# Optimization experiments

Hardware: AMD Instinct MI355X
Metric: run time of the kernel (lower is better)

## Reference

```python
import jax, jax.numpy as jnp
import numpy as np

D_MODEL = 256
NHEAD = 8
HEAD_DIM = D_MODEL // NHEAD
NLAYERS = 8
LAYER_NAMES = ('self', 'cross', 'self', 'cross', 'self', 'cross', 'self', 'cross')
LN_EPS = 1e-5
ATTN_EPS = 1e-6


def _layernorm(x, g, b):
    mu = jnp.mean(x, axis=-1, keepdims=True)
    var = jnp.mean(jnp.square(x - mu), axis=-1, keepdims=True)
    return (x - mu) * jax.lax.rsqrt(var + LN_EPS) * g + b


def _encoder_layer(x, source, Wq, Wk, Wv, Wm, W1, W2, g1, b1, g2, b2):
    # x: [N, L, C], source: [N, S, C]; weights stored [in, out] so y = x @ W
    bs, L, C = x.shape
    S = source.shape[1]
    q = (x @ Wq).reshape(bs, L, NHEAD, HEAD_DIM)
    k = (source @ Wk).reshape(bs, S, NHEAD, HEAD_DIM)
    v = (source @ Wv).reshape(bs, S, NHEAD, HEAD_DIM)
    # LoFTR LinearAttention: feature map elu(x)+1, O(N d^2) kernelized attention
    Q = jax.nn.elu(q) + 1.0
    K = jax.nn.elu(k) + 1.0
    v_n = v / S  # normalize values by kv length for numerical stability
    KV = jnp.einsum('nshd,nshv->nhdv', K, v_n)            # [N,H,D,D]
    Z = 1.0 / (jnp.einsum('nlhd,nhd->nlh', Q, K.sum(axis=1)) + ATTN_EPS)
    msg = jnp.einsum('nlhd,nhdv,nlh->nlhv', Q, KV, Z) * S  # [N,L,H,D]
    msg = msg.reshape(bs, L, C) @ Wm
    msg = _layernorm(msg, g1, b1)
    h = jnp.concatenate([x, msg], axis=-1)                 # [N,L,2C]
    h = jax.nn.relu(h @ W1) @ W2
    h = _layernorm(h, g2, b2)
    return x + h


def _transformer(feat0, feat1, Wq, Wk, Wv, Wm, W1, W2, g1, b1, g2, b2):
    for i, name in enumerate(LAYER_NAMES):
        p = (Wq[i], Wk[i], Wv[i], Wm[i], W1[i], W2[i], g1[i], b1[i], g2[i], b2[i])
        if name == 'self':
            feat0 = _encoder_layer(feat0, feat0, *p)
            feat1 = _encoder_layer(feat1, feat1, *p)
        else:  # cross
            new0 = _encoder_layer(feat0, feat1, *p)
            feat1 = _encoder_layer(feat1, feat0, *p)
            feat0 = new0
    return feat0, feat1


def setup_inputs() -> dict:
    key = jax.random.key(0)
    ks = jax.random.split(key, 8)
    N, L = 4, 4800
    feat0 = jax.random.normal(ks[0], (N, L, D_MODEL), jnp.float32)
    feat1 = jax.random.normal(ks[1], (N, L, D_MODEL), jnp.float32)
    xav = lambda k, fi, fo: jax.random.normal(k, (NLAYERS, fi, fo), jnp.float32) * float(np.sqrt(2.0 / (fi + fo)))
    Wq = xav(ks[2], D_MODEL, D_MODEL)
    Wk = xav(ks[3], D_MODEL, D_MODEL)
    Wv = xav(ks[4], D_MODEL, D_MODEL)
    Wm = xav(ks[5], D_MODEL, D_MODEL)
    W1 = xav(ks[6], 2 * D_MODEL, 2 * D_MODEL)
    W2 = xav(ks[7], 2 * D_MODEL, D_MODEL)
    g1 = jnp.ones((NLAYERS, D_MODEL), jnp.float32)
    b1 = jnp.zeros((NLAYERS, D_MODEL), jnp.float32)
    g2 = jnp.ones((NLAYERS, D_MODEL), jnp.float32)
    b2 = jnp.zeros((NLAYERS, D_MODEL), jnp.float32)
    return dict(feat0=feat0, feat1=feat1, Wq=Wq, Wk=Wk, Wv=Wv, Wm=Wm,
                W1=W1, W2=W2, g1=g1, b1=b1, g2=g2, b2=b2)


def reference(feat0, feat1, Wq, Wk, Wv, Wm, W1, W2, g1, b1, g2, b2):
    return _transformer(feat0, feat1, Wq, Wk, Wv, Wm, W1, W2, g1, b1, g2, b2)
```

## Files before the change

### kernel.cpp

```cpp
#include <hip/hip_runtime.h>
#include <math.h>

#define RTOT 19200
#define RALL 38400
#define CDIM 256
#define SLEN 4800
#define NB 8
#define NHEAD 8
#define SEG 25
#define SCHUNK 192

typedef __attribute__((ext_vector_type(8))) short short8v;
typedef __attribute__((ext_vector_type(4))) float f32x4;

__device__ __forceinline__ ushort f2b(float f) {
    unsigned u = __float_as_uint(f);
    unsigned r = (u + 0x7FFFu + ((u >> 16) & 1u)) >> 16;
    return (ushort)r;
}
__device__ __forceinline__ float b2f(ushort u) {
    return __uint_as_float(((unsigned)u) << 16);
}

__device__ __forceinline__ float elu1(float v) { return v > 0.0f ? v + 1.0f : __expf(v); }

__device__ __forceinline__ void gload16(const void* g, void* l) {
    __builtin_amdgcn_global_load_lds((const __attribute__((address_space(1))) void*)g,
                                     (__attribute__((address_space(3))) void*)l, 16, 0, 0);
}

__global__ __launch_bounds__(256) void qkv_gemm(
    const ushort* __restrict__ A, const ushort* __restrict__ Bt,
    ushort* __restrict__ Oq, ushort* __restrict__ Ok, ushort* __restrict__ Ov)
{
    __shared__ __align__(16) ushort As[2][128 * 32];
    __shared__ __align__(16) ushort Bs[2][128 * 32];
    const int t = threadIdx.x;
    const int wave = t >> 6, lane = t & 63;
    const int bm = blockIdx.y * 128, bn = blockIdx.x * 128;
    const int wr = wave >> 1, wc = wave & 1;
    const int lr = lane & 15, lk = (lane >> 4) * 8;

    const int srow = t >> 2;
    const int sgrp = ((t & 3) * 8) ^ ((srow & 3) * 8);
    const ushort* bAr = A + (size_t)(bm + srow) * 256 + sgrp;
    const ushort* bBr = Bt + (size_t)(bn + srow) * 256 + sgrp;

    const f32x4 z4 = {0.f, 0.f, 0.f, 0.f};
    f32x4 acc[4][4];
    #pragma unroll
    for (int m = 0; m < 4; ++m)
        #pragma unroll
        for (int n = 0; n < 4; ++n) acc[m][n] = z4;

    auto stage = [&](int k0, int b) {
        char* la = (char*)As[b] + wave * 1024;
        char* lb = (char*)Bs[b] + wave * 1024;
        gload16(bAr + k0, la);
        gload16(bAr + k0 + 64 * 256, la + 4096);
        gload16(bBr + k0, lb);
        gload16(bBr + k0 + 64 * 256, lb + 4096);
    };

    stage(0, 0);
    __syncthreads();
    int cur = 0;
    for (int k0 = 0; k0 < 256; k0 += 32) {
        if (k0 + 32 < 256) stage(k0 + 32, cur ^ 1);
        short8v af[4], bfr[4];
        #pragma unroll
        for (int m = 0; m < 4; ++m) {
            const int r = wr * 64 + m * 16 + lr;
            af[m] = *(const short8v*)&As[cur][r * 32 + (lk ^ ((r & 3) * 8))];
        }
        #pragma unroll
        for (int n = 0; n < 4; ++n) {
            const int r = wc * 64 + n * 16 + lr;
            bfr[n] = *(const short8v*)&Bs[cur][r * 32 + (lk ^ ((r & 3) * 8))];
        }
        #pragma unroll
        for (int m = 0; m < 4; ++m)
            #pragma unroll
            for (int n = 0; n < 4; ++n)
                acc[m][n] = __builtin_amdgcn_mfma_f32_16x16x32_bf16(af[m], bfr[n], acc[m][n], 0, 0, 0);
        __syncthreads();
        cur ^= 1;
    }

    const int orow = bm + wr * 64 + (lane >> 4) * 4;
    const int ocol = bn + wc * 64 + lr;
    #pragma unroll
    for (int m = 0; m < 4; ++m)
        #pragma unroll
        for (int n = 0; n < 4; ++n)
            #pragma unroll
            for (int j = 0; j < 4; ++j) {
                const float v = acc[m][n][j];
                const size_t row = (size_t)(orow + m * 16 + j);
                const int col = ocol + n * 16;
                const int seg = col >> 8, c = col & 255;
                ushort* dst = seg == 0 ? Oq : (seg == 1 ? Ok : Ov);
                dst[row * 256 + c] = f2b(seg < 2 ? elu1(v) : v);
            }
}

__global__ __launch_bounds__(256) void w1_gemm(
    const ushort* __restrict__ A, const ushort* __restrict__ A2,
    const ushort* __restrict__ Bt, ushort* __restrict__ O)
{
    __shared__ __align__(16) ushort As[2][128 * 32];
    __shared__ __align__(16) ushort Bs[2][128 * 32];
    const int t = threadIdx.x;
    const int wave = t >> 6, lane = t & 63;
    const int bm = blockIdx.y * 128, bn = blockIdx.x * 128;
    const int wr = wave >> 1, wc = wave & 1;
    const int lr = lane & 15, lk = (lane >> 4) * 8;

    const int srow = t >> 2;
    const int sgrp = ((t & 3) * 8) ^ ((srow & 3) * 8);
    const ushort* bAr = A + (size_t)(bm + srow) * 256 + sgrp;
    const ushort* bA2r = A2 + (size_t)(bm + srow) * 256 + sgrp;
    const ushort* bBr = Bt + (size_t)(bn + srow) * 512 + sgrp;

    const f32x4 z4 = {0.f, 0.f, 0.f, 0.f};
    f32x4 acc[4][4];
    #pragma unroll
    for (int m = 0; m < 4; ++m)
        #pragma unroll
        for (int n = 0; n < 4; ++n) acc[m][n] = z4;

    auto stage = [&](int k0, int b) {
        char* la = (char*)As[b] + wave * 1024;
        char* lb = (char*)Bs[b] + wave * 1024;
        const ushort* ga = (k0 < 256) ? (bAr + k0) : (bA2r + (k0 - 256));
        gload16(ga, la);
        gload16(ga + 64 * 256, la + 4096);
        gload16(bBr + k0, lb);
        gload16(bBr + k0 + (size_t)64 * 512, lb + 4096);
    };

    stage(0, 0);
    __syncthreads();
    int cur = 0;
    for (int k0 = 0; k0 < 512; k0 += 32) {
        if (k0 + 32 < 512) stage(k0 + 32, cur ^ 1);
        short8v af[4], bfr[4];
        #pragma unroll
        for (int m = 0; m < 4; ++m) {
            const int r = wr * 64 + m * 16 + lr;
            af[m] = *(const short8v*)&As[cur][r * 32 + (lk ^ ((r & 3) * 8))];
        }
        #pragma unroll
        for (int n = 0; n < 4; ++n) {
            const int r = wc * 64 + n * 16 + lr;
            bfr[n] = *(const short8v*)&Bs[cur][r * 32 + (lk ^ ((r & 3) * 8))];
        }
        #pragma unroll
        for (int m = 0; m < 4; ++m)
            #pragma unroll
            for (int n = 0; n < 4; ++n)
                acc[m][n] = __builtin_amdgcn_mfma_f32_16x16x32_bf16(af[m], bfr[n], acc[m][n], 0, 0, 0);
        __syncthreads();
        cur ^= 1;
    }

    const int orow = bm + wr * 64 + (lane >> 4) * 4;
    const int ocol = bn + wc * 64 + lr;
    #pragma unroll
    for (int m = 0; m < 4; ++m)
        #pragma unroll
        for (int n = 0; n < 4; ++n)
            #pragma unroll
            for (int j = 0; j < 4; ++j) {
                const float v = acc[m][n][j];
                O[(size_t)(orow + m * 16 + j) * 512 + ocol + n * 16] = f2b(v > 0.f ? v : 0.f);
            }
}

__global__ __launch_bounds__(256) void gemm_ln32(
    const ushort* __restrict__ A, int lda,
    const ushort* __restrict__ Bt,
    const float* __restrict__ g, const float* __restrict__ bb,
    const float* __restrict__ rx0, const float* __restrict__ rx1,
    float* __restrict__ outf, ushort* __restrict__ outb, int K)
{
    __shared__ __align__(16) ushort As[2][32 * 32];
    __shared__ __align__(16) ushort Bs[2][256 * 32];
    __shared__ float red[2][4][32];
    const int t = threadIdx.x;
    const int wave = t >> 6, lane = t & 63;
    const int bm = blockIdx.x * 32;
    const int lr = lane & 15, kg = lane >> 4, lk = kg * 8;

    const int srow = t >> 2;
    const int sg = ((t & 3) * 8) ^ ((srow & 3) * 8);
    const ushort* aP = A + (size_t)(bm + srow) * lda + sg;
    const ushort* bP = Bt + (size_t)srow * K + sg;
    const size_t b64 = (size_t)64 * K;

    auto stage = [&](int k0, int b) {
        if (srow < 32) gload16(aP + k0, (char*)As[b] + wave * 1024);
        char* lb = (char*)Bs[b] + wave * 1024;
        gload16(bP + k0, lb);
        gload16(bP + k0 + b64, lb + 4096);
        gload16(bP + k0 + 2 * b64, lb + 8192);
        gload16(bP + k0 + 3 * b64, lb + 12288);
    };

    const f32x4 z4 = {0.f, 0.f, 0.f, 0.f};
    f32x4 acc[2][4];
    #pragma unroll
    for (int m = 0; m < 2; ++m)
        #pragma unroll
        for (int n = 0; n < 4; ++n) acc[m][n] = z4;

    stage(0, 0);
    __syncthreads();
    int cur = 0;
    for (int k0 = 0; k0 < K; k0 += 32) {
        if (k0 + 32 < K) stage(k0 + 32, cur ^ 1);
        short8v af[2], bfr[4];
        #pragma unroll
        for (int m = 0; m < 2; ++m) {
            const int r = m * 16 + lr;
            af[m] = *(const short8v*)&As[cur][r * 32 + (lk ^ ((r & 3) * 8))];
        }
        #pragma unroll
        for (int n = 0; n < 4; ++n) {
            const int r = wave * 64 + n * 16 + lr;
            bfr[n] = *(const short8v*)&Bs[cur][r * 32 + (lk ^ ((r & 3) * 8))];
        }
        #pragma unroll
        for (int m = 0; m < 2; ++m)
            #pragma unroll
            for (int n = 0; n < 4; ++n)
                acc[m][n] = __builtin_amdgcn_mfma_f32_16x16x32_bf16(af[m], bfr[n], acc[m][n], 0, 0, 0);
        __syncthreads();
        cur ^= 1;
    }

    #pragma unroll
    for (int m = 0; m < 2; ++m)
        #pragma unroll
        for (int j = 0; j < 4; ++j) {
            float s = 0.f, q = 0.f;
            #pragma unroll
            for (int n = 0; n < 4; ++n) { const float v = acc[m][n][j]; s += v; q += v * v; }
            #pragma unroll
            for (int mk = 1; mk < 16; mk <<= 1) { s += __shfl_xor(s, mk); q += __shfl_xor(q, mk); }
            if (lr == 0) {
                red[0][wave][m * 16 + kg * 4 + j] = s;
                red[1][wave][m * 16 + kg * 4 + j] = q;
            }
        }
    __syncthreads();

    float gv[4], bv[4];
    #pragma unroll
    for (int n = 0; n < 4; ++n) {
        const int col = wave * 64 + n * 16 + lr;
        gv[n] = g[col]; bv[n] = bb[col];
    }
    const float* rxb = (bm < RTOT) ? rx0 + (size_t)bm * CDIM : rx1 + (size_t)(bm - RTOT) * CDIM;

    #pragma unroll
    for (int m = 0; m < 2; ++m)
        #pragma unroll
        for (int j = 0; j < 4; ++j) {
            const int row = m * 16 + kg * 4 + j;
            const float tot = red[0][0][row] + red[0][1][row] + red[0][2][row] + red[0][3][row];
            const float tq  = red[1][0][row] + red[1][1][row] + red[1][2][row] + red[1][3][row];
            const float mu = tot * (1.0f / 256.0f);
            const float var = tq * (1.0f / 256.0f) - mu * mu;
            const float inv = rsqrtf(var + 1e-5f);
            const size_t go = (size_t)(bm + row) * CDIM;
            #pragma unroll
            for (int n = 0; n < 4; ++n) {
                const int col = wave * 64 + n * 16 + lr;
                float val = (acc[m][n][j] - mu) * inv * gv[n] + bv[n];
                val += rxb[(size_t)row * CDIM + col];
                outf[go + col] = val;
                outb[go + col] = f2b(val);
            }
        }
}

__global__ __launch_bounds__(256) void attn_wm_ln(
    const ushort* __restrict__ Qb, const ushort* __restrict__ KVbT,
    const ushort* __restrict__ Ksb, const ushort* __restrict__ WmT,
    const float* __restrict__ g, const float* __restrict__ bb,
    ushort* __restrict__ mln, int xorv)
{
    __shared__ __align__(16) ushort Ms[32 * 256];
    __shared__ __align__(16) ushort Bs[2][256 * 32];
    __shared__ float red[2][4][32];
    const int t = threadIdx.x, wave = t >> 6, lane = t & 63;
    const int bm = blockIdx.x * 32;
    const int n = bm / SLEN, src = n ^ xorv;
    const int lr = lane & 15, kg = lane >> 4, lk = kg * 8;
    const f32x4 z4 = {0.f, 0.f, 0.f, 0.f};

    const int srow = t >> 2;
    const int sg = ((t & 3) * 8) ^ ((srow & 3) * 8);
    const ushort* bP = WmT + (size_t)srow * 256 + sg;
    auto stageB = [&](int k0, int b) {
        char* lb = (char*)Bs[b] + wave * 1024;
        gload16(bP + k0, lb);
        gload16(bP + k0 + 64 * 256, lb + 4096);
        gload16(bP + k0 + 128 * 256, lb + 8192);
        gload16(bP + k0 + 192 * 256, lb + 12288);
    };
    stageB(0, 0);

    {
        const int rw = (wave & 1) * 16;
        const size_t qrow = ((size_t)bm + rw + lr) * CDIM;
        char* mb = (char*)Ms;
        for (int h = (wave >> 1); h < NHEAD; h += 2) {
            const short8v af = *(const short8v*)&Qb[qrow + h * 32 + kg * 8];
            const ushort* bbp = KVbT + ((size_t)(src * NHEAD + h)) * 1024;
            const short8v b0 = *(const short8v*)&bbp[lr * 32 + kg * 8];
            const short8v b1 = *(const short8v*)&bbp[(16 + lr) * 32 + kg * 8];
            const short8v bz = *(const short8v*)&Ksb[((size_t)(src * NHEAD + h)) * 512 + lr * 32 + kg * 8];
            f32x4 a0 = __builtin_amdgcn_mfma_f32_16x16x32_bf16(af, b0, z4, 0, 0, 0);
            f32x4 a1 = __builtin_amdgcn_mfma_f32_16x16x32_bf16(af, b1, z4, 0, 0, 0);
            f32x4 az = __builtin_amdgcn_mfma_f32_16x16x32_bf16(af, bz, z4, 0, 0, 0);
            #pragma unroll
            for (int j = 0; j < 4; ++j) {
                const float zj = __shfl(az[j], lane & 48);
                const float rz = 1.0f / (zj + 1e-6f);
                const int orow = rw + kg * 4 + j;
                const int swz = (orow & 7) << 4;
                *(ushort*)(mb + ((orow * 512 + (h * 32 + lr) * 2) ^ swz)) = f2b(a0[j] * rz);
                *(ushort*)(mb + ((orow * 512 + (h * 32 + 16 + lr) * 2) ^ swz)) = f2b(a1[j] * rz);
            }
        }
    }
    __syncthreads();

    f32x4 acc[2][4];
    #pragma unroll
    for (int m = 0; m < 2; ++m)
        #pragma unroll
        for (int nn = 0; nn < 4; ++nn) acc[m][nn] = z4;

    int cur = 0;
    for (int k0 = 0; k0 < 256; k0 += 32) {
        if (k0 + 32 < 256) stageB(k0 + 32, cur ^ 1);
        short8v af[2], bfr[4];
        #pragma unroll
        for (int m = 0; m < 2; ++m) {
            const int r = m * 16 + lr;
            af[m] = *(const short8v*)((char*)Ms + ((r * 512 + k0 * 2 + kg * 16) ^ ((r & 7) << 4)));
        }
        #pragma unroll
        for (int nn = 0; nn < 4; ++nn) {
            const int r = wave * 64 + nn * 16 + lr;
            bfr[nn] = *(const short8v*)&Bs[cur][r * 32 + (lk ^ ((r & 3) * 8))];
        }
        #pragma unroll
        for (int m = 0; m < 2; ++m)
            #pragma unroll
            for (int nn = 0; nn < 4; ++nn)
                acc[m][nn] = __builtin_amdgcn_mfma_f32_16x16x32_bf16(af[m], bfr[nn], acc[m][nn], 0, 0, 0);
        __syncthreads();
        cur ^= 1;
    }

    #pragma unroll
    for (int m = 0; m < 2; ++m)
        #pragma unroll
        for (int j = 0; j < 4; ++j) {
            float s = 0.f, q = 0.f;
            #pragma unroll
            for (int nn = 0; nn < 4; ++nn) { const float v = acc[m][nn][j]; s += v; q += v * v; }
            #pragma unroll
            for (int mk = 1; mk < 16; mk <<= 1) { s += __shfl_xor(s, mk); q += __shfl_xor(q, mk); }
            if (lr == 0) {
                red[0][wave][m * 16 + kg * 4 + j] = s;
                red[1][wave][m * 16 + kg * 4 + j] = q;
            }
        }
    __syncthreads();

    float gv[4], bv[4];
    #pragma unroll
    for (int nn = 0; nn < 4; ++nn) {
        const int col = wave * 64 + nn * 16 + lr;
        gv[nn] = g[col]; bv[nn] = bb[col];
    }
    #pragma unroll
    for (int m = 0; m < 2; ++m)
        #pragma unroll
        for (int j = 0; j < 4; ++j) {
            const int row = m * 16 + kg * 4 + j;
            const float tot = red[0][0][row] + red[0][1][row] + red[0][2][row] + red[0][3][row];
            const float tq  = red[1][0][row] + red[1][1][row] + red[1][2][row] + red[1][3][row];
            const float mu = tot * (1.0f / 256.0f);
            const float var = tq * (1.0f / 256.0f) - mu * mu;
            const float inv = rsqrtf(var + 1e-5f);
            const size_t go = (size_t)(bm + row) * CDIM;
            #pragma unroll
            for (int nn = 0; nn < 4; ++nn) {
                const int col = wave * 64 + nn * 16 + lr;
                mln[go + col] = f2b((acc[m][nn][j] - mu) * inv * gv[nn] + bv[nn]);
            }
        }
}

__global__ __launch_bounds__(256) void wconv_t(
    const float* __restrict__ src, ushort* __restrict__ dst, int R, int C, size_t dstride)
{
    __shared__ float tile[32][33];
    const int l = blockIdx.z;
    const int r0 = blockIdx.y * 32, c0 = blockIdx.x * 32;
    const int tx = threadIdx.x & 31, ty = threadIdx.x >> 5;
    const float* s = src + (size_t)l * R * C;
    ushort* d = dst + (size_t)l * dstride;
    for (int i = ty; i < 32; i += 8) tile[i][tx] = s[(size_t)(r0 + i) * C + c0 + tx];
    __syncthreads();
    for (int i = ty; i < 32; i += 8) d[(size_t)(c0 + i) * R + r0 + tx] = f2b(tile[tx][i]);
}

__global__ __launch_bounds__(256) void kv_part_k(
    const ushort* __restrict__ Kb, const ushort* __restrict__ Vb,
    float* __restrict__ KVp, float* __restrict__ Ksp)
{
    const int blk = blockIdx.x;
    const int seg = blk % SEG;
    const int h = (blk / SEG) % NHEAD;
    const int n = blk / (SEG * NHEAD);
    const int s0 = seg * SCHUNK;
    __shared__ float Ks[16][32];
    __shared__ float Vs[16][32];
    const int t = threadIdx.x;
    const int rr = t >> 4, c2 = (t & 15) * 2;
    const int d = t >> 3, v0 = (t & 7) * 4;
    float a0 = 0, a1 = 0, a2 = 0, a3 = 0, ksum = 0;
    for (int c = 0; c < SCHUNK; c += 16) {
        const size_t off = ((size_t)(n * SLEN + s0 + c + rr)) * CDIM + h * 32 + c2;
        const ushort2 ku = *(const ushort2*)&Kb[off];
        const ushort2 vu = *(const ushort2*)&Vb[off];
        Ks[rr][c2] = b2f(ku.x); Ks[rr][c2 + 1] = b2f(ku.y);
        Vs[rr][c2] = b2f(vu.x); Vs[rr][c2 + 1] = b2f(vu.y);
        __syncthreads();
        #pragma unroll
        for (int q = 0; q < 16; ++q) {
            const float kd = Ks[q][d];
            a0 += kd * Vs[q][v0 + 0];
            a1 += kd * Vs[q][v0 + 1];
            a2 += kd * Vs[q][v0 + 2];
            a3 += kd * Vs[q][v0 + 3];
        }
        if (t < 32) {
            #pragma unroll
            for (int q = 0; q < 16; ++q) ksum += Ks[q][t];
        }
        __syncthreads();
    }
    float* kvp = KVp + ((size_t)((n * NHEAD + h) * SEG + seg)) * 1024;
    kvp[t * 4 + 0] = a0;
    kvp[t * 4 + 1] = a1;
    kvp[t * 4 + 2] = a2;
    kvp[t * 4 + 3] = a3;
    if (t < 32) Ksp[((size_t)((n * NHEAD + h) * SEG + seg)) * 32 + t] = ksum;
}

__global__ __launch_bounds__(256) void kv_reduce_k(
    const float* __restrict__ KVp, const float* __restrict__ Ksp,
    ushort* __restrict__ KVbT, ushort* __restrict__ Ksb)
{
    const int nh = blockIdx.x;
    const int t = threadIdx.x;
    #pragma unroll
    for (int i = 0; i < 4; ++i) {
        const int idx = t * 4 + i;
        const int v = idx >> 5, d = idx & 31;
        float s = 0;
        for (int seg = 0; seg < SEG; ++seg)
            s += KVp[((size_t)(nh * SEG + seg)) * 1024 + d * 32 + v];
        KVbT[(size_t)nh * 1024 + idx] = f2b(s);
    }
    #pragma unroll
    for (int i = 0; i < 2; ++i) {
        const int idx = t * 2 + i;
        const int c = idx >> 5, d = idx & 31;
        float s = 0;
        if (c == 0)
            for (int seg = 0; seg < SEG; ++seg)
                s += Ksp[((size_t)(nh * SEG + seg)) * 32 + d];
        Ksb[(size_t)nh * 512 + idx] = f2b(s);
    }
}

__global__ __launch_bounds__(256) void cvt_in_k(const float* __restrict__ src, ushort* __restrict__ dst) {
    const size_t i = ((size_t)blockIdx.x * 256 + threadIdx.x) * 4;
    const float4 v = *(const float4*)&src[i];
    ushort4 ob = make_ushort4(f2b(v.x), f2b(v.y), f2b(v.z), f2b(v.w));
    *(ushort4*)&dst[i] = ob;
}

struct Ws {
    float *xf, *KVp, *Ksp;
    ushort *xb, *Qb, *Kb, *Vb, *h1b, *KVbT, *Ksb;
    ushort *WqkvT, *WmT, *W1T, *W2T;
};

static void layer_pass(const float* rx0, const float* rx1, float* destf, int xorv,
                       const ushort* WqkvT, const ushort* WmT,
                       const ushort* W1T, const ushort* W2T,
                       const float* g1, const float* b1,
                       const float* g2, const float* b2,
                       const Ws& w, hipStream_t stream)
{
    const dim3 blk(256);
    qkv_gemm<<<dim3(6, RALL / 128), blk, 0, stream>>>(w.xb, WqkvT, w.Qb, w.Kb, w.Vb);
    kv_part_k<<<dim3(NB * NHEAD * SEG), blk, 0, stream>>>(w.Kb, w.Vb, w.KVp, w.Ksp);
    kv_reduce_k<<<dim3(NB * NHEAD), blk, 0, stream>>>(w.KVp, w.Ksp, w.KVbT, w.Ksb);
    attn_wm_ln<<<dim3(RALL / 32), blk, 0, stream>>>(
        w.Qb, w.KVbT, w.Ksb, WmT, g1, b1, w.Kb, xorv);
    w1_gemm<<<dim3(4, RALL / 128), blk, 0, stream>>>(w.xb, w.Kb, W1T, w.h1b);
    gemm_ln32<<<dim3(RALL / 32), blk, 0, stream>>>(
        w.h1b, 512, W2T, g2, b2, rx0, rx1, destf, w.xb, 512);
}

extern "C" void kernel_launch(void* const* d_in, const int* in_sizes, int n_in,
                              void* d_out, int out_size, void* d_ws, size_t ws_size,
                              hipStream_t stream) {
    (void)in_sizes; (void)n_in; (void)out_size; (void)ws_size;
    const float* f0in = (const float*)d_in[0];
    const float* f1in = (const float*)d_in[1];
    const float* WqA = (const float*)d_in[2];
    const float* WkA = (const float*)d_in[3];
    const float* WvA = (const float*)d_in[4];
    const float* WmA = (const float*)d_in[5];
    const float* W1A = (const float*)d_in[6];
    const float* W2A = (const float*)d_in[7];
    const float* g1A = (const float*)d_in[8];
    const float* b1A = (const float*)d_in[9];
    const float* g2A = (const float*)d_in[10];
    const float* b2A = (const float*)d_in[11];

    float* outf = (float*)d_out;
    const size_t RC = (size_t)RTOT * CDIM;
    const size_t RAC = (size_t)RALL * CDIM;

    float* wsf = (float*)d_ws;
    Ws w;
    w.xf  = wsf;
    w.KVp = w.xf + RAC;
    w.Ksp = w.KVp + (size_t)64 * SEG * 1024;
    ushort* p = (ushort*)(w.Ksp + 64 * SEG * 32);
    w.xb = p;   p += RAC;
    w.Qb = p;   p += RAC;
    w.Kb = p;   p += RAC;
    w.Vb = p;   p += RAC;
    w.h1b = p;  p += (size_t)RALL * 512;
    w.KVbT = p; p += 64 * 1024;
    w.Ksb = p;  p += 64 * 512;
    w.WqkvT = p; p += (size_t)8 * 768 * 256;
    w.WmT = p;  p += (size_t)8 * 256 * 256;
    w.W1T = p;  p += (size_t)8 * 512 * 512;
    w.W2T = p;  p += (size_t)8 * 512 * 256;

    const dim3 blk(256);
    wconv_t<<<dim3(8, 8, 8), blk, 0, stream>>>(WqA, w.WqkvT,             256, 256, 768 * 256);
    wconv_t<<<dim3(8, 8, 8), blk, 0, stream>>>(WkA, w.WqkvT + 256 * 256, 256, 256, 768 * 256);
    wconv_t<<<dim3(8, 8, 8), blk, 0, stream>>>(WvA, w.WqkvT + 512 * 256, 256, 256, 768 * 256);
    wconv_t<<<dim3(8, 8, 8), blk, 0, stream>>>(WmA, w.WmT, 256, 256, 65536);
    wconv_t<<<dim3(16, 16, 8), blk, 0, stream>>>(W1A, w.W1T, 512, 512, 262144);
    wconv_t<<<dim3(8, 16, 8), blk, 0, stream>>>(W2A, w.W2T, 512, 256, 131072);

    cvt_in_k<<<dim3(RC / 1024), blk, 0, stream>>>(f0in, w.xb);
    cvt_in_k<<<dim3(RC / 1024), blk, 0, stream>>>(f1in, w.xb + RC);

    for (int l = 0; l < 8; ++l) {
        const int xorv = (l & 1) ? 4 : 0;
        const float* rx0 = (l == 0) ? f0in : w.xf;
        const float* rx1 = (l == 0) ? f1in : w.xf + RC;
        float* destf = (l == 7) ? outf : w.xf;
        layer_pass(rx0, rx1, destf, xorv,
                   w.WqkvT + (size_t)l * 768 * 256,
                   w.WmT + (size_t)l * 65536,
                   w.W1T + (size_t)l * 262144,
                   w.W2T + (size_t)l * 131072,
                   g1A + l * 256, b1A + l * 256, g2A + l * 256, b2A + l * 256,
                   w, stream);
    }
}
```

Before: 1.439 ms.

## Keep residual stream in bf16 only and stage full A rows in LDS for FFN GEMMs

Drops the fp32 residual copy: the W2+LayerNorm kernel now reads the residual from the bf16 activation buffer and writes fp32 output only on the last layer, which cuts fp32 read/write traffic per layer. The W1 GEMM moves to 64-row tiles that load the whole 512-wide A row (x concatenated with the message) into swizzled LDS once, and the W2 kernel does the same with a 32-row A block, so only B is double-buffered. The cost is that the residual accumulates in bf16 across all eight layers, which loses precision, and the W1 kernel now uses more LDS with a smaller M tile.

```diff
diff --git a/kernel.cpp b/kernel.cpp
--- a/kernel.cpp
+++ b/kernel.cpp
@@ -104,59 +104,61 @@
             }
 }
 
-__global__ __launch_bounds__(256) void w1_gemm(
-    const ushort* __restrict__ A, const ushort* __restrict__ A2,
+__global__ __launch_bounds__(256) void w1_gemm64(
+    const ushort* __restrict__ xb, const ushort* __restrict__ mln,
     const ushort* __restrict__ Bt, ushort* __restrict__ O)
 {
-    __shared__ __align__(16) ushort As[2][128 * 32];
+    __shared__ __align__(16) ushort A512[64 * 512];
     __shared__ __align__(16) ushort Bs[2][128 * 32];
-    const int t = threadIdx.x;
-    const int wave = t >> 6, lane = t & 63;
-    const int bm = blockIdx.y * 128, bn = blockIdx.x * 128;
+    const int t = threadIdx.x, wave = t >> 6, lane = t & 63;
+    const int bm = blockIdx.y * 64, bn = blockIdx.x * 128;
     const int wr = wave >> 1, wc = wave & 1;
-    const int lr = lane & 15, lk = (lane >> 4) * 8;
+    const int lr = lane & 15, kg = lane >> 4, lk = kg * 8;
+    const f32x4 z4 = {0.f, 0.f, 0.f, 0.f};
+
+    #pragma unroll
+    for (int i = 0; i < 16; ++i) {
+        const int row = i * 4 + wave;
+        const int gl = lane ^ (row & 7);
+        const ushort* src = (gl < 32) ? (xb + (size_t)(bm + row) * 256 + gl * 8)
+                                      : (mln + (size_t)(bm + row) * 256 + (gl - 32) * 8);
+        gload16(src, (char*)A512 + row * 1024);
+    }
 
     const int srow = t >> 2;
-    const int sgrp = ((t & 3) * 8) ^ ((srow & 3) * 8);
-    const ushort* bAr = A + (size_t)(bm + srow) * 256 + sgrp;
-    const ushort* bA2r = A2 + (size_t)(bm + srow) * 256 + sgrp;
-    const ushort* bBr = Bt + (size_t)(bn + srow) * 512 + sgrp;
-
-    const f32x4 z4 = {0.f, 0.f, 0.f, 0.f};
-    f32x4 acc[4][4];
-    #pragma unroll
-    for (int m = 0; m < 4; ++m)
+    const int sg = ((t & 3) * 8) ^ ((srow & 3) * 8);
+    const ushort* bP = Bt + (size_t)(bn + srow) * 512 + sg;
+    auto stageB = [&](int k0, int b) {
+        char* lb = (char*)Bs[b] + wave * 1024;
+        gload16(bP + k0, lb);
+        gload16(bP + k0 + (size_t)64 * 512, lb + 4096);
+    };
+
+    f32x4 acc[2][4];
+    #pragma unroll
+    for (int m = 0; m < 2; ++m)
         #pragma unroll
         for (int n = 0; n < 4; ++n) acc[m][n] = z4;
 
-    auto stage = [&](int k0, int b) {
-        char* la = (char*)As[b] + wave * 1024;
-        char* lb = (char*)Bs[b] + wave * 1024;
-        const ushort* ga = (k0 < 256) ? (bAr + k0) : (bA2r + (k0 - 256));
-        gload16(ga, la);
-        gload16(ga + 64 * 256, la + 4096);
-        gload16(bBr + k0, lb);
-        gload16(bBr + k0 + (size_t)64 * 512, lb + 4096);
-    };
-
-    stage(0, 0);
+    stageB(0, 0);
     __syncthreads();
     int cur = 0;
     for (int k0 = 0; k0 < 512; k0 += 32) {
-        if (k0 + 32 < 512) stage(k0 + 32, cur ^ 1);
-        short8v af[4], bfr[4];
-        #pragma unroll
-        for (int m = 0; m < 4; ++m) {
-            const int r = wr * 64 + m * 16 + lr;
-            af[m] = *(const short8v*)&As[cur][r * 32 + (lk ^ ((r & 3) * 8))];
+        if (k0 + 32 < 512) stageB(k0 + 32, cur ^ 1);
+        short8v af[2], bfr[4];
+        #pragma unroll
+        for (int m = 0; m < 2; ++m) {
+            const int r = wr * 32 + m * 16 + lr;
+            const int q = (k0 >> 3) + kg;
+            af[m] = *(const short8v*)((char*)A512 + r * 1024 + ((q ^ (r & 7)) << 4));
         }
         #pragma unroll
         for (int n = 0; n < 4; ++n) {
-            const int r = wc * 64 + n * 16 + lr;
-            bfr[n] = *(const short8v*)&Bs[cur][r * 32 + (lk ^ ((r & 3) * 8))];
-        }
-        #pragma unroll
-        for (int m = 0; m < 4; ++m)
+            const int rB = wc * 64 + n * 16 + lr;
+            bfr[n] = *(const short8v*)&Bs[cur][rB * 32 + (lk ^ ((rB & 3) * 8))];
+        }
+        #pragma unroll
+        for (int m = 0; m < 2; ++m)
             #pragma unroll
             for (int n = 0; n < 4; ++n)
                 acc[m][n] = __builtin_amdgcn_mfma_f32_16x16x32_bf16(af[m], bfr[n], acc[m][n], 0, 0, 0);
@@ -164,10 +166,10 @@
         cur ^= 1;
     }
 
-    const int orow = bm + wr * 64 + (lane >> 4) * 4;
+    const int orow = bm + wr * 32 + kg * 4;
     const int ocol = bn + wc * 64 + lr;
     #pragma unroll
-    for (int m = 0; m < 4; ++m)
+    for (int m = 0; m < 2; ++m)
         #pragma unroll
         for (int n = 0; n < 4; ++n)
             #pragma unroll
@@ -177,58 +179,62 @@
             }
 }
 
-__global__ __launch_bounds__(256) void gemm_ln32(
-    const ushort* __restrict__ A, int lda,
+__global__ __launch_bounds__(256) void w2_ln(
+    const ushort* __restrict__ A,
     const ushort* __restrict__ Bt,
     const float* __restrict__ g, const float* __restrict__ bb,
-    const float* __restrict__ rx0, const float* __restrict__ rx1,
-    float* __restrict__ outf, ushort* __restrict__ outb, int K)
-{
-    __shared__ __align__(16) ushort As[2][32 * 32];
+    const ushort* __restrict__ resid,
+    float* __restrict__ outf,
+    ushort* __restrict__ outb)
+{
+    __shared__ __align__(16) ushort A512[32 * 512];
     __shared__ __align__(16) ushort Bs[2][256 * 32];
     __shared__ float red[2][4][32];
-    const int t = threadIdx.x;
-    const int wave = t >> 6, lane = t & 63;
+    const int t = threadIdx.x, wave = t >> 6, lane = t & 63;
     const int bm = blockIdx.x * 32;
     const int lr = lane & 15, kg = lane >> 4, lk = kg * 8;
+    const f32x4 z4 = {0.f, 0.f, 0.f, 0.f};
+
+    #pragma unroll
+    for (int i = 0; i < 8; ++i) {
+        const int row = i * 4 + wave;
+        const int gl = lane ^ (row & 7);
+        gload16(A + (size_t)(bm + row) * 512 + gl * 8, (char*)A512 + row * 1024);
+    }
 
     const int srow = t >> 2;
     const int sg = ((t & 3) * 8) ^ ((srow & 3) * 8);
-    const ushort* aP = A + (size_t)(bm + srow) * lda + sg;
-    const ushort* bP = Bt + (size_t)srow * K + sg;
-    const size_t b64 = (size_t)64 * K;
-
-    auto stage = [&](int k0, int b) {
-        if (srow < 32) gload16(aP + k0, (char*)As[b] + wave * 1024);
+    const ushort* bP = Bt + (size_t)srow * 512 + sg;
+    auto stageB = [&](int k0, int b) {
         char* lb = (char*)Bs[b] + wave * 1024;
         gload16(bP + k0, lb);
-        gload16(bP + k0 + b64, lb + 4096);
-        gload16(bP + k0 + 2 * b64, lb + 8192);
-        gload16(bP + k0 + 3 * b64, lb + 12288);
+        gload16(bP + k0 + (size_t)64 * 512, lb + 4096);
+        gload16(bP + k0 + (size_t)128 * 512, lb + 8192);
+        gload16(bP + k0 + (size_t)192 * 512, lb + 12288);
     };
 
-    const f32x4 z4 = {0.f, 0.f, 0.f, 0.f};
     f32x4 acc[2][4];
     #pragma unroll
     for (int m = 0; m < 2; ++m)
         #pragma unroll
         for (int n = 0; n < 4; ++n) acc[m][n] = z4;
 
-    stage(0, 0);
+    stageB(0, 0);
     __syncthreads();
     int cur = 0;
-    for (int k0 = 0; k0 < K; k0 += 32) {
-        if (k0 + 32 < K) stage(k0 + 32, cur ^ 1);
+    for (int k0 = 0; k0 < 512; k0 += 32) {
+        if (k0 + 32 < 512) stageB(k0 + 32, cur ^ 1);
         short8v af[2], bfr[4];
         #pragma unroll
         for (int m = 0; m < 2; ++m) {
             const int r = m * 16 + lr;
-            af[m] = *(const short8v*)&As[cur][r * 32 + (lk ^ ((r & 3) * 8))];
+            const int q = (k0 >> 3) + kg;
+            af[m] = *(const short8v*)((char*)A512 + r * 1024 + ((q ^ (r & 7)) << 4));
         }
         #pragma unroll
         for (int n = 0; n < 4; ++n) {
-            const int r = wave * 64 + n * 16 + lr;
-            bfr[n] = *(const short8v*)&Bs[cur][r * 32 + (lk ^ ((r & 3) * 8))];
+            const int rB = wave * 64 + n * 16 + lr;
+            bfr[n] = *(const short8v*)&Bs[cur][rB * 32 + (lk ^ ((rB & 3) * 8))];
         }
         #pragma unroll
         for (int m = 0; m < 2; ++m)
@@ -261,7 +267,7 @@
         const int col = wave * 64 + n * 16 + lr;
         gv[n] = g[col]; bv[n] = bb[col];
     }
-    const float* rxb = (bm < RTOT) ? rx0 + (size_t)bm * CDIM : rx1 + (size_t)(bm - RTOT) * CDIM;
+    const ushort* rxb = resid + (size_t)bm * CDIM;
 
     #pragma unroll
     for (int m = 0; m < 2; ++m)
@@ -278,8 +284,8 @@
             for (int n = 0; n < 4; ++n) {
                 const int col = wave * 64 + n * 16 + lr;
                 float val = (acc[m][n][j] - mu) * inv * gv[n] + bv[n];
-                val += rxb[(size_t)row * CDIM + col];
-                outf[go + col] = val;
+                val += b2f(rxb[(size_t)row * CDIM + col]);
+                if (outf) outf[go + col] = val;
                 outb[go + col] = f2b(val);
             }
         }
@@ -501,12 +507,12 @@
 }
 
 struct Ws {
-    float *xf, *KVp, *Ksp;
+    float *KVp, *Ksp;
     ushort *xb, *Qb, *Kb, *Vb, *h1b, *KVbT, *Ksb;
     ushort *WqkvT, *WmT, *W1T, *W2T;
 };
 
-static void layer_pass(const float* rx0, const float* rx1, float* destf, int xorv,
+static void layer_pass(float* destf, int xorv,
                        const ushort* WqkvT, const ushort* WmT,
                        const ushort* W1T, const ushort* W2T,
                        const float* g1, const float* b1,
@@ -519,9 +525,9 @@
     kv_reduce_k<<<dim3(NB * NHEAD), blk, 0, stream>>>(w.KVp, w.Ksp, w.KVbT, w.Ksb);
     attn_wm_ln<<<dim3(RALL / 32), blk, 0, stream>>>(
         w.Qb, w.KVbT, w.Ksb, WmT, g1, b1, w.Kb, xorv);
-    w1_gemm<<<dim3(4, RALL / 128), blk, 0, stream>>>(w.xb, w.Kb, W1T, w.h1b);
-    gemm_ln32<<<dim3(RALL / 32), blk, 0, stream>>>(
-        w.h1b, 512, W2T, g2, b2, rx0, rx1, destf, w.xb, 512);
+    w1_gemm64<<<dim3(4, RALL / 64), blk, 0, stream>>>(w.xb, w.Kb, W1T, w.h1b);
+    w2_ln<<<dim3(RALL / 32), blk, 0, stream>>>(
+        w.h1b, W2T, g2, b2, w.xb, destf, w.xb);
 }
 
 extern "C" void kernel_launch(void* const* d_in, const int* in_sizes, int n_in,
@@ -547,8 +553,7 @@
 
     float* wsf = (float*)d_ws;
     Ws w;
-    w.xf  = wsf;
-    w.KVp = w.xf + RAC;
+    w.KVp = wsf;
     w.Ksp = w.KVp + (size_t)64 * SEG * 1024;
     ushort* p = (ushort*)(w.Ksp + 64 * SEG * 32);
     w.xb = p;   p += RAC;
@@ -576,10 +581,8 @@
 
     for (int l = 0; l < 8; ++l) {
         const int xorv = (l & 1) ? 4 : 0;
-        const float* rx0 = (l == 0) ? f0in : w.xf;
-        const float* rx1 = (l == 0) ? f1in : w.xf + RC;
-        float* destf = (l == 7) ? outf : w.xf;
-        layer_pass(rx0, rx1, destf, xorv,
+        float* destf = (l == 7) ? outf : nullptr;
+        layer_pass(destf, xorv,
                    w.WqkvT + (size_t)l * 768 * 256,
                    w.WmT + (size_t)l * 65536,
                    w.W1T + (size_t)l * 262144,
```

New measurement: 1.622 ms. 1.13x slower.
